# Kernel optimization log

Measured on AMD Instinct MI355X. Metric: run time of the kernel, lower is better.

Reference implementation:

```python
import jax, jax.numpy as jnp
import numpy as np

B, SQ, SKV, D = 32, 1024, 8192, 64

def setup_inputs() -> dict:
    key = jax.random.key(0)
    kq, kk, kv = jax.random.split(key, 3)
    return {
        "q_local": jax.random.normal(kq, (B, SQ, D), dtype=jnp.float32),
        "k_local": jax.random.normal(kk, (B, SKV, D), dtype=jnp.float32),
        "v_local": jax.random.normal(kv, (B, SKV, D), dtype=jnp.float32),
    }

def reference(q_local, k_local, v_local):
    # Ring attention with online softmax over all ranks' K/V blocks is
    # mathematically identical to unscaled softmax(Q K^T) V over the full KV.
    scores = jnp.einsum("bqd,bkd->bqk", q_local, k_local)  # [B, SQ, SKV]
    weights = jax.nn.softmax(scores, axis=-1)              # stable (max-subtract)
    out = jnp.einsum("bqk,bkd->bqd", weights, v_local)
    return out.astype(q_local.dtype)
```

## Files before the change

kernel.cpp:

```cpp
#include <hip/hip_runtime.h>


#define NBATCH 32
#define SQL 1024
#define SKVL 8192
#define DH 64
#define BM 128
#define BN 64
#define KSTR 72
#define VSTR 72
#define NSPL 3

typedef _Float16 half8 __attribute__((ext_vector_type(8)));
typedef __fp16 fp16x2 __attribute__((ext_vector_type(2)));
typedef float floatx16 __attribute__((ext_vector_type(16)));
typedef float floatx4 __attribute__((ext_vector_type(4)));
typedef unsigned int uint4v __attribute__((ext_vector_type(4)));
typedef unsigned int uint2v __attribute__((ext_vector_type(2)));

union F8U { uint4v u; half8 h; };

#if __has_builtin(__builtin_amdgcn_exp2f)
#define EXP2F(x) __builtin_amdgcn_exp2f(x)
#else
#define EXP2F(x) exp2f(x)
#endif

#define WGBAR() do {                                        \
    asm volatile("s_waitcnt lgkmcnt(0)" ::: "memory");      \
    __builtin_amdgcn_s_barrier();                           \
    asm volatile("" ::: "memory");                          \
  } while (0)

static __device__ __forceinline__ unsigned pk2(float a, float b) {
#if __has_builtin(__builtin_amdgcn_cvt_pkrtz)
  fp16x2 h = __builtin_amdgcn_cvt_pkrtz(a, b);
  return __builtin_bit_cast(unsigned, h);
#else
  union { _Float16 h[2]; unsigned u; } r;
  r.h[0] = (_Float16)a; r.h[1] = (_Float16)b; return r.u;
#endif
}

#if __has_builtin(__builtin_amdgcn_permlane32_swap)
#define HAVE_PL32 1
static __device__ __forceinline__ void pl32(unsigned& a, unsigned& b) {
  uint2v r = __builtin_amdgcn_permlane32_swap(a, b, false, false);
  a = r[0]; b = r[1];
}
#else
#define HAVE_PL32 0
#endif

template<int NSPLIT>
__global__ __launch_bounds__(256, 3)
void ring_attn(const float* __restrict__ q, const float* __restrict__ k,
               const float* __restrict__ v, float* __restrict__ out,
               float* __restrict__ pO, float* __restrict__ pM, float* __restrict__ pL)
{
  constexpr int TT = SKVL / BN;
  __shared__ _Float16 Kl[2][BN * KSTR];
  __shared__ _Float16 Vt[2][DH * VSTR];

  const int tid  = threadIdx.x;
  const int lane = tid & 63;
  const int wv   = tid >> 6;
  const int l31  = lane & 31;
  const int hb   = lane >> 5;
  const int b8   = hb * 8;

  int split, batch, qb;
  if (NSPLIT == 3) {
    split = blockIdx.x % 3;
    batch = (blockIdx.x / 3) & 31;
    qb    = blockIdx.x / 96;
  } else {
    split = 0;
    batch = blockIdx.x & 31;
    qb    = blockIdx.x >> 5;
  }
  const int t0 = (split * TT) / NSPLIT;
  const int t1 = ((split + 1) * TT) / NSPLIT;

  const float* kp = k + (size_t)batch * SKVL * DH;
  const float* vp = v + (size_t)batch * SKVL * DH;

  const float* qp = q + ((size_t)batch * SQL + qb * BM + wv * 32 + l31) * DH;
  half8 qf[4];
#pragma unroll
  for (int kt = 0; kt < 4; ++kt) {
    float4 a = *(const float4*)(qp + kt * 16 + b8);
    float4 c = *(const float4*)(qp + kt * 16 + b8 + 4);
    float xs[8] = {a.x, a.y, a.z, a.w, c.x, c.y, c.z, c.w};
#pragma unroll
    for (int j = 0; j < 8; ++j)
      qf[kt][j] = (_Float16)(xs[j] * 1.44269504088896340736f);
  }

  const int krt = tid >> 4;
  const int kc  = (tid & 15) * 4;
  const int vnr = 2 * (tid & 31);
  const int vcg = 8 * (tid >> 5);

  float4 gk[4], ga0, ga1, gb0, gb1;
  {
    const float* kt_ = kp + (size_t)t0 * BN * DH;
    const float* vt_ = vp + (size_t)t0 * BN * DH;
#pragma unroll
    for (int it = 0; it < 4; ++it)
      gk[it] = *(const float4*)(kt_ + (size_t)(krt + it * 16) * DH + kc);
    ga0 = *(const float4*)(vt_ + (size_t)vnr * DH + vcg);
    ga1 = *(const float4*)(vt_ + (size_t)vnr * DH + vcg + 4);
    gb0 = *(const float4*)(vt_ + (size_t)(vnr + 1) * DH + vcg);
    gb1 = *(const float4*)(vt_ + (size_t)(vnr + 1) * DH + vcg + 4);
  }

  floatx16 accO[2];
#pragma unroll
  for (int i = 0; i < 2; ++i)
#pragma unroll
    for (int r = 0; r < 16; ++r) accO[i][r] = 0.f;
  float m_run = -3.0e38f, l_run = 0.f;

  int buf = 0;
  for (int tile = t0; tile < t1; ++tile) {
    _Float16* Kb = Kl[buf];
    _Float16* Vb = Vt[buf];

#pragma unroll
    for (int it = 0; it < 4; ++it) {
      uint2 w2 = make_uint2(pk2(gk[it].x, gk[it].y), pk2(gk[it].z, gk[it].w));
      *(uint2*)&Kb[(krt + it * 16) * KSTR + kc] = w2;
    }
    WGBAR();

    {
      float av[8] = {ga0.x, ga0.y, ga0.z, ga0.w, ga1.x, ga1.y, ga1.z, ga1.w};
      float bv[8] = {gb0.x, gb0.y, gb0.z, gb0.w, gb1.x, gb1.y, gb1.z, gb1.w};
#pragma unroll
      for (int i = 0; i < 8; ++i)
        *(unsigned*)&Vb[(vcg + i) * VSTR + vnr] = pk2(av[i], bv[i]);
    }

    if (tile + 1 < t1) {
      const float* kn = kp + (size_t)(tile + 1) * BN * DH;
      const float* vn = vp + (size_t)(tile + 1) * BN * DH;
#pragma unroll
      for (int it = 0; it < 4; ++it)
        gk[it] = *(const float4*)(kn + (size_t)(krt + it * 16) * DH + kc);
      ga0 = *(const float4*)(vn + (size_t)vnr * DH + vcg);
      ga1 = *(const float4*)(vn + (size_t)vnr * DH + vcg + 4);
      gb0 = *(const float4*)(vn + (size_t)(vnr + 1) * DH + vcg);
      gb1 = *(const float4*)(vn + (size_t)(vnr + 1) * DH + vcg + 4);
    }

    floatx16 st[2];
#pragma unroll
    for (int t = 0; t < 2; ++t)
#pragma unroll
      for (int r = 0; r < 16; ++r) st[t][r] = 0.f;
    __builtin_amdgcn_s_setprio(1);
#pragma unroll
    for (int kt = 0; kt < 4; ++kt) {
#pragma unroll
      for (int t = 0; t < 2; ++t) {
        half8 kf = *(const half8*)&Kb[(t * 32 + l31) * KSTR + kt * 16 + b8];
        st[t] = __builtin_amdgcn_mfma_f32_32x32x16_f16(kf, qf[kt], st[t], 0, 0, 0);
      }
    }
    __builtin_amdgcn_s_setprio(0);

    float r0, r1, r2, r3;
    {
      float a[16];
#pragma unroll
      for (int r = 0; r < 16; ++r) a[r] = fmaxf(st[0][r], st[1][r]);
      r0 = fmaxf(fmaxf(a[0],  a[1]),  fmaxf(a[2],  a[3]));
      r1 = fmaxf(fmaxf(a[4],  a[5]),  fmaxf(a[6],  a[7]));
      r2 = fmaxf(fmaxf(a[8],  a[9]),  fmaxf(a[10], a[11]));
      r3 = fmaxf(fmaxf(a[12], a[13]), fmaxf(a[14], a[15]));
    }
    float mx = fmaxf(fmaxf(r0, r1), fmaxf(r2, r3));
    mx = fmaxf(mx, __shfl_xor(mx, 32, 64));
    float m_new = fmaxf(m_run, mx);
    float alpha = EXP2F(m_run - m_new);
    m_run = m_new;
#pragma unroll
    for (int t = 0; t < 2; ++t)
#pragma unroll
      for (int r = 0; r < 16; ++r)
        st[t][r] = EXP2F(st[t][r] - m_new);
    float sm[16];
#pragma unroll
    for (int r = 0; r < 16; ++r) sm[r] = st[0][r] + st[1][r];
#pragma unroll
    for (int s = 8; s >= 1; s >>= 1)
#pragma unroll
      for (int r = 0; r < 8; ++r)
        if (r < s) sm[r] += sm[r + s];
    float sum = sm[0] + __shfl_xor(sm[0], 32, 64);
    l_run = alpha * l_run + sum;

    if (__any(alpha != 1.0f)) {
#pragma unroll
      for (int r = 0; r < 16; ++r) {
        int row = (r & 3) + 8 * (r >> 2) + 4 * hb;
        float ar = __shfl(alpha, row, 64);
        accO[0][r] *= ar;
        accO[1][r] *= ar;
      }
    }

    WGBAR();

    __builtin_amdgcn_s_setprio(1);
#pragma unroll
    for (int t = 0; t < 2; ++t) {
      unsigned P01 = pk2(st[t][0],  st[t][1]);
      unsigned P23 = pk2(st[t][2],  st[t][3]);
      unsigned P45 = pk2(st[t][4],  st[t][5]);
      unsigned P67 = pk2(st[t][6],  st[t][7]);
      unsigned P89 = pk2(st[t][8],  st[t][9]);
      unsigned PAB = pk2(st[t][10], st[t][11]);
      unsigned PCD = pk2(st[t][12], st[t][13]);
      unsigned PEF = pk2(st[t][14], st[t][15]);
      F8U fe, fo;
#if HAVE_PL32
      pl32(P01, P45); fe.u[0] = P01; fe.u[2] = P45;
      pl32(P23, P67); fe.u[1] = P23; fe.u[3] = P67;
      pl32(P89, PCD); fo.u[0] = P89; fo.u[2] = PCD;
      pl32(PAB, PEF); fo.u[1] = PAB; fo.u[3] = PEF;
#else
      unsigned x01 = __shfl_xor(P01, 32, 64), x23 = __shfl_xor(P23, 32, 64);
      unsigned x45 = __shfl_xor(P45, 32, 64), x67 = __shfl_xor(P67, 32, 64);
      unsigned x89 = __shfl_xor(P89, 32, 64), xAB = __shfl_xor(PAB, 32, 64);
      unsigned xCD = __shfl_xor(PCD, 32, 64), xEF = __shfl_xor(PEF, 32, 64);
      fe.u = uint4v{hb ? x45 : P01, hb ? x67 : P23, hb ? P45 : x01, hb ? P67 : x23};
      fo.u = uint4v{hb ? xCD : P89, hb ? xEF : PAB, hb ? PCD : x89, hb ? PEF : xAB};
#endif
#pragma unroll
      for (int ds = 0; ds < 2; ++ds) {
        half8 vf0 = *(const half8*)&Vb[(ds * 32 + l31) * VSTR + (2 * t) * 16 + b8];
        accO[ds] = __builtin_amdgcn_mfma_f32_32x32x16_f16(fe.h, vf0, accO[ds], 0, 0, 0);
        half8 vf1 = *(const half8*)&Vb[(ds * 32 + l31) * VSTR + (2 * t + 1) * 16 + b8];
        accO[ds] = __builtin_amdgcn_mfma_f32_32x32x16_f16(fo.h, vf1, accO[ds], 0, 0, 0);
      }
    }
    __builtin_amdgcn_s_setprio(0);
    buf ^= 1;
  }

  const int rowbase = batch * SQL + qb * BM + wv * 32;
  if (NSPLIT == 1) {
    float linv = 1.0f / l_run;
    float* op = out + (size_t)rowbase * DH;
#pragma unroll
    for (int r = 0; r < 16; ++r) {
      int row = (r & 3) + 8 * (r >> 2) + 4 * hb;
      float lr = __shfl(linv, row, 64);
      op[(size_t)row * DH + l31]      = accO[0][r] * lr;
      op[(size_t)row * DH + 32 + l31] = accO[1][r] * lr;
    }
  } else {
    float* po = pO + ((size_t)split * NBATCH * SQL + rowbase) * DH;
#pragma unroll
    for (int r = 0; r < 16; ++r) {
      int row = (r & 3) + 8 * (r >> 2) + 4 * hb;
      po[(size_t)row * DH + l31]      = accO[0][r];
      po[(size_t)row * DH + 32 + l31] = accO[1][r];
    }
    if (hb == 0) {
      pM[(size_t)split * NBATCH * SQL + rowbase + l31] = m_run;
      pL[(size_t)split * NBATCH * SQL + rowbase + l31] = l_run;
    }
  }
}

__global__ __launch_bounds__(256)
void merge3(const float* __restrict__ pO, const float* __restrict__ pM,
            const float* __restrict__ pL, float* __restrict__ out)
{
  const int i4   = blockIdx.x * 256 + threadIdx.x;
  const int rowg = i4 >> 4;
  const size_t PLANE4 = (size_t)NBATCH * SQL * DH / 4;
  const int    RPL    = NBATCH * SQL;
  float m0 = pM[rowg], m1 = pM[RPL + rowg], m2 = pM[2 * RPL + rowg];
  float mx = fmaxf(fmaxf(m0, m1), m2);
  float w0 = EXP2F(m0 - mx), w1 = EXP2F(m1 - mx), w2 = EXP2F(m2 - mx);
  float l = w0 * pL[rowg] + w1 * pL[RPL + rowg] + w2 * pL[2 * RPL + rowg];
  float li = 1.0f / l;
  const floatx4* p0 = (const floatx4*)pO;
  floatx4 o0 = p0[i4], o1 = p0[PLANE4 + i4], o2 = p0[2 * PLANE4 + i4];
  floatx4 o;
#pragma unroll
  for (int j = 0; j < 4; ++j)
    o[j] = (w0 * o0[j] + w1 * o1[j] + w2 * o2[j]) * li;
  ((floatx4*)out)[i4] = o;
}

extern "C" void kernel_launch(void* const* d_in, const int* in_sizes, int n_in,
                              void* d_out, int out_size, void* d_ws, size_t ws_size,
                              hipStream_t stream) {
  (void)in_sizes; (void)n_in; (void)out_size;
  const float* q = (const float*)d_in[0];
  const float* k = (const float*)d_in[1];
  const float* v = (const float*)d_in[2];
  float* out = (float*)d_out;

  const size_t PLANE = (size_t)NBATCH * SQL * DH;
  const size_t RPL   = (size_t)NBATCH * SQL;
  const size_t need  = (3 * PLANE + 6 * RPL) * sizeof(float);

  if (ws_size >= need) {
    float* pO = (float*)d_ws;
    float* pM = pO + 3 * PLANE;
    float* pL = pM + 3 * RPL;
    ring_attn<NSPL><<<dim3(768), dim3(256), 0, stream>>>(q, k, v, nullptr, pO, pM, pL);
    merge3<<<dim3((NBATCH * SQL * DH) / 1024), dim3(256), 0, stream>>>(pO, pM, pL, out);
  } else {
    ring_attn<1><<<dim3(256), dim3(256), 0, stream>>>(q, k, v, out, nullptr, nullptr, nullptr);
  }
}
```

Before: 236.0 us.

## Fold max-subtraction into MFMA init, lazy rescale, row sums via MFMA

The score accumulator now starts at the negated running max, so the subtraction happens inside the QK MFMA. The running max is only raised when some row exceeds it by more than a threshold (lazy rescaling, FA4-style). Row sums of P are computed by an extra MFMA against a ones vector instead of a register reduction tree. This removes per-tile VALU max/sub/sum work and most rescale branches, at the cost of two extra MFMAs per tile and weaker overflow margin in fp16 P (values up to 2^8).

```diff
diff --git a/kernel.cpp b/kernel.cpp
--- a/kernel.cpp
+++ b/kernel.cpp
@@ -10,6 +10,7 @@
 #define KSTR 72
 #define VSTR 72
 #define NSPL 3
+#define RESCALE_THR 8.0f
 
 typedef _Float16 half8 __attribute__((ext_vector_type(8)));
 typedef __fp16 fp16x2 __attribute__((ext_vector_type(2)));
@@ -97,6 +98,10 @@
       qf[kt][j] = (_Float16)(xs[j] * 1.44269504088896340736f);
   }
 
+  half8 ones;
+#pragma unroll
+  for (int j = 0; j < 8; ++j) ones[j] = (_Float16)1.0f;
+
   const int krt = tid >> 4;
   const int kc  = (tid & 15) * 4;
   const int vnr = 2 * (tid & 31);
@@ -115,12 +120,14 @@
     gb1 = *(const float4*)(vt_ + (size_t)(vnr + 1) * DH + vcg + 4);
   }
 
-  floatx16 accO[2];
+  floatx16 accO[2], accL;
 #pragma unroll
   for (int i = 0; i < 2; ++i)
 #pragma unroll
     for (int r = 0; r < 16; ++r) accO[i][r] = 0.f;
-  float m_run = -3.0e38f, l_run = 0.f;
+#pragma unroll
+  for (int r = 0; r < 16; ++r) accL[r] = 0.f;
+  float m_run = 0.f;
 
   int buf = 0;
   for (int tile = t0; tile < t1; ++tile) {
@@ -154,11 +161,12 @@
       gb1 = *(const float4*)(vn + (size_t)(vnr + 1) * DH + vcg + 4);
     }
 
+    const float negm = -m_run;
     floatx16 st[2];
 #pragma unroll
     for (int t = 0; t < 2; ++t)
 #pragma unroll
-      for (int r = 0; r < 16; ++r) st[t][r] = 0.f;
+      for (int r = 0; r < 16; ++r) st[t][r] = negm;
     __builtin_amdgcn_s_setprio(1);
 #pragma unroll
     for (int kt = 0; kt < 4; ++kt) {
@@ -170,46 +178,42 @@
     }
     __builtin_amdgcn_s_setprio(0);
 
-    float r0, r1, r2, r3;
+    float mx;
     {
       float a[16];
 #pragma unroll
       for (int r = 0; r < 16; ++r) a[r] = fmaxf(st[0][r], st[1][r]);
-      r0 = fmaxf(fmaxf(a[0],  a[1]),  fmaxf(a[2],  a[3]));
-      r1 = fmaxf(fmaxf(a[4],  a[5]),  fmaxf(a[6],  a[7]));
-      r2 = fmaxf(fmaxf(a[8],  a[9]),  fmaxf(a[10], a[11]));
-      r3 = fmaxf(fmaxf(a[12], a[13]), fmaxf(a[14], a[15]));
-    }
-    float mx = fmaxf(fmaxf(r0, r1), fmaxf(r2, r3));
+      float c0 = fmaxf(fmaxf(a[0],  a[1]),  fmaxf(a[2],  a[3]));
+      float c1 = fmaxf(fmaxf(a[4],  a[5]),  fmaxf(a[6],  a[7]));
+      float c2 = fmaxf(fmaxf(a[8],  a[9]),  fmaxf(a[10], a[11]));
+      float c3 = fmaxf(fmaxf(a[12], a[13]), fmaxf(a[14], a[15]));
+      mx = fmaxf(fmaxf(c0, c1), fmaxf(c2, c3));
+    }
     mx = fmaxf(mx, __shfl_xor(mx, 32, 64));
-    float m_new = fmaxf(m_run, mx);
-    float alpha = EXP2F(m_run - m_new);
-    m_run = m_new;
-#pragma unroll
-    for (int t = 0; t < 2; ++t)
-#pragma unroll
-      for (int r = 0; r < 16; ++r)
-        st[t][r] = EXP2F(st[t][r] - m_new);
-    float sm[16];
-#pragma unroll
-    for (int r = 0; r < 16; ++r) sm[r] = st[0][r] + st[1][r];
-#pragma unroll
-    for (int s = 8; s >= 1; s >>= 1)
-#pragma unroll
-      for (int r = 0; r < 8; ++r)
-        if (r < s) sm[r] += sm[r + s];
-    float sum = sm[0] + __shfl_xor(sm[0], 32, 64);
-    l_run = alpha * l_run + sum;
-
-    if (__any(alpha != 1.0f)) {
+
+    if (__any(mx > RESCALE_THR)) {
+      float d  = fmaxf(mx, 0.f);
+      m_run += d;
+      float al = EXP2F(-d);
+#pragma unroll
+      for (int t = 0; t < 2; ++t)
+#pragma unroll
+        for (int r = 0; r < 16; ++r) st[t][r] -= d;
 #pragma unroll
       for (int r = 0; r < 16; ++r) {
         int row = (r & 3) + 8 * (r >> 2) + 4 * hb;
-        float ar = __shfl(alpha, row, 64);
+        float ar = __shfl(al, row, 64);
         accO[0][r] *= ar;
         accO[1][r] *= ar;
+        accL[r]    *= ar;
       }
     }
+
+#pragma unroll
+    for (int t = 0; t < 2; ++t)
+#pragma unroll
+      for (int r = 0; r < 16; ++r)
+        st[t][r] = EXP2F(st[t][r]);
 
     WGBAR();
 
@@ -238,6 +242,8 @@
       fe.u = uint4v{hb ? x45 : P01, hb ? x67 : P23, hb ? P45 : x01, hb ? P67 : x23};
       fo.u = uint4v{hb ? xCD : P89, hb ? xEF : PAB, hb ? PCD : x89, hb ? PEF : xAB};
 #endif
+      accL = __builtin_amdgcn_mfma_f32_32x32x16_f16(fe.h, ones, accL, 0, 0, 0);
+      accL = __builtin_amdgcn_mfma_f32_32x32x16_f16(fo.h, ones, accL, 0, 0, 0);
 #pragma unroll
       for (int ds = 0; ds < 2; ++ds) {
         half8 vf0 = *(const half8*)&Vb[(ds * 32 + l31) * VSTR + (2 * t) * 16 + b8];
@@ -252,12 +258,11 @@
 
   const int rowbase = batch * SQL + qb * BM + wv * 32;
   if (NSPLIT == 1) {
-    float linv = 1.0f / l_run;
     float* op = out + (size_t)rowbase * DH;
 #pragma unroll
     for (int r = 0; r < 16; ++r) {
       int row = (r & 3) + 8 * (r >> 2) + 4 * hb;
-      float lr = __shfl(linv, row, 64);
+      float lr = 1.0f / accL[r];
       op[(size_t)row * DH + l31]      = accO[0][r] * lr;
       op[(size_t)row * DH + 32 + l31] = accO[1][r] * lr;
     }
@@ -269,9 +274,14 @@
       po[(size_t)row * DH + l31]      = accO[0][r];
       po[(size_t)row * DH + 32 + l31] = accO[1][r];
     }
-    if (hb == 0) {
+    if (hb == 0)
       pM[(size_t)split * NBATCH * SQL + rowbase + l31] = m_run;
-      pL[(size_t)split * NBATCH * SQL + rowbase + l31] = l_run;
+    if (l31 == 0) {
+#pragma unroll
+      for (int r = 0; r < 16; ++r) {
+        int row = (r & 3) + 8 * (r >> 2) + 4 * hb;
+        pL[(size_t)split * NBATCH * SQL + rowbase + row] = accL[r];
+      }
     }
   }
 }
```

New measurement: 232.0 us. No clear change (-1.7%).
